# Optimization experiments

Hardware: AMD Instinct MI355X
Metric: run time of the kernel (lower is better)

Reference implementation:

```python
import jax, jax.numpy as jnp
import numpy as np

B, CIN, COUT, H, W = 8, 256, 256, 64, 64
WBIT = 4  # weight_bit


def _fake_quant_sym(w, bits):
    # Symmetric per-tensor fake quantization with straight-through rounding.
    n = 2.0 ** (bits - 1) - 1
    mag = jax.lax.stop_gradient(
        jnp.maximum(jnp.abs(jnp.min(w)), jnp.abs(jnp.max(w))))
    s = jnp.maximum(mag, 1e-8) / n
    q = w / s
    q = q + jax.lax.stop_gradient(jnp.round(q) - q)  # STE round
    return jnp.clip(q, -n - 1, n) * s


def _conv3x3(x, w, b):
    out = jax.lax.conv_general_dilated(
        x, w, window_strides=(1, 1), padding=((1, 1), (1, 1)),
        dimension_numbers=('NCHW', 'OIHW', 'NCHW'))
    return out + b[None, :, None, None]


def _bilinear_gather(x, py, px):
    # x: [B,C,H,W]; py, px: [B,K,Ho,Wo] float sample coords. Zero outside.
    b, c, h, w = x.shape
    y0 = jnp.floor(py)
    x0 = jnp.floor(px)
    wy = (py - y0)[:, None]  # [B,1,K,Ho,Wo]
    wx = (px - x0)[:, None]
    flat = x.reshape(b, c, h * w)

    def gather(yi, xi):
        valid = (yi >= 0) & (yi <= h - 1) & (xi >= 0) & (xi <= w - 1)
        yc = jnp.clip(yi, 0, h - 1).astype(jnp.int32)
        xc = jnp.clip(xi, 0, w - 1).astype(jnp.int32)
        idx = (yc * w + xc).reshape(b, -1)  # [B, K*Ho*Wo]
        g = jax.vmap(lambda f, i: f[:, i])(flat, idx)  # [B,C,K*Ho*Wo]
        g = g.reshape(b, c, *yi.shape[1:])  # [B,C,K,Ho,Wo]
        return g * valid[:, None].astype(x.dtype)

    v00 = gather(y0, x0)
    v01 = gather(y0, x0 + 1)
    v10 = gather(y0 + 1, x0)
    v11 = gather(y0 + 1, x0 + 1)
    return (v00 * (1 - wy) * (1 - wx) + v01 * (1 - wy) * wx
            + v10 * wy * (1 - wx) + v11 * wy * wx)


def setup_inputs() -> dict:
    key = jax.random.key(0)
    ks = jax.random.split(key, 4)
    return {
        'x': jax.random.normal(ks[0], (B, CIN, H, W), jnp.float32),
        'w_off': jax.random.normal(ks[1], (2, CIN, 3, 3), jnp.float32) * 0.01,
        'b_off': jnp.zeros((2,), jnp.float32),
        'w_scale': jax.random.normal(ks[2], (1, CIN, 3, 3), jnp.float32) * 0.01,
        'b_scale': jnp.ones((1,), jnp.float32),
        'w_dcn': jax.random.normal(ks[3], (COUT, CIN, 3, 3), jnp.float32)
                 / np.float32(np.sqrt(CIN * 9)),
        'b_dcn': jnp.zeros((COUT,), jnp.float32),
    }


def reference(x, w_off, b_off, w_scale, b_scale, w_dcn, b_dcn):
    # Fake-quantize all conv weights (per-tensor symmetric, STE).
    w_off_q = _fake_quant_sym(w_off, WBIT)
    w_scale_q = _fake_quant_sym(w_scale, WBIT)
    w_dcn_q = _fake_quant_sym(w_dcn, WBIT)

    # Per-location offset (dy,dx) and positive-bounded scale.
    off = _conv3x3(x, w_off_q, b_off)                 # [B,2,H,W]
    scale = jax.nn.relu(_conv3x3(x, w_scale_q, b_scale))  # [B,1,H,W]

    # Kernel anchor grid (row-major 3x3, (ry,rx) in {-1,0,1}).
    ry = jnp.array([-1, -1, -1, 0, 0, 0, 1, 1, 1], jnp.float32)
    rx = jnp.array([-1, 0, 1, -1, 0, 1, -1, 0, 1], jnp.float32)
    ii = jnp.arange(H, dtype=jnp.float32)[None, None, :, None]
    jj = jnp.arange(W, dtype=jnp.float32)[None, None, None, :]
    # sample pos = base + anchor + [offset + anchor*(scale-1)] = base + anchor*scale + offset
    py = ii + ry[None, :, None, None] * scale + off[:, 0:1]   # [B,9,H,W]
    px = jj + rx[None, :, None, None] * scale + off[:, 1:2]

    sampled = _bilinear_gather(x, py, px)             # [B,C,9,H,W]
    out = jnp.einsum('bckhw,ock->bohw', sampled, w_dcn_q.reshape(COUT, CIN, 9))
    return out + b_dcn[None, :, None, None]
```

## Files before the change

kernel.cpp:

```cpp
#include <hip/hip_runtime.h>

#define BB   8
#define CIN  256
#define COUT 256
#define HH   64
#define WW   64
#define HW   (HH*WW)
#define KT   9
#define KTOT (CIN*KT)
#define WR   12
#define RSTR 65
#define CSTR 786

typedef short short8 __attribute__((ext_vector_type(8)));
typedef float f32x4  __attribute__((ext_vector_type(4)));
typedef float f32x2  __attribute__((ext_vector_type(2)));
typedef float f32x16 __attribute__((ext_vector_type(16)));
union FragU { short8 s8; unsigned u[4]; uint4 u4; };

#define WS_OFF     0
#define WS_SCALE   65536
#define WS_PART    98304
#define WS_SDCN    98368
#define WS_WOFFQ   98372
#define WS_WSCALEQ 102980
#define WS_B       105284

#define USE_FP8_HW __has_builtin(__builtin_amdgcn_cvt_pk_f32_fp8)

__device__ __forceinline__ float fq(float w, float s) {
    float q = rintf(w / s);
    q = fminf(fmaxf(q, -8.f), 7.f);
    return q * s;
}

__device__ __forceinline__ unsigned short f2bf(float f) {
    unsigned u = __float_as_uint(f);
    return (unsigned short)((u + 0x7fffu + ((u >> 16) & 1u)) >> 16);
}

__global__ __launch_bounds__(256) void prep_kernel(const float* __restrict__ w_dcn,
                                                   const float* __restrict__ w_off,
                                                   const float* __restrict__ w_scale,
                                                   float* __restrict__ ws) {
    __shared__ float red[256];
    const int bx = blockIdx.x, tid = threadIdx.x;
    if (bx < 64) {
        float m = 0.f;
        const float* p = w_dcn + bx * 9216;
#pragma unroll
        for (int k = 0; k < 36; ++k) m = fmaxf(m, fabsf(p[tid + k * 256]));
        red[tid] = m;
        __syncthreads();
        for (int s = 128; s > 0; s >>= 1) {
            if (tid < s) red[tid] = fmaxf(red[tid], red[tid + s]);
            __syncthreads();
        }
        if (tid == 0) ws[WS_PART + bx] = red[0];
    } else {
        const float* src = (bx == 64) ? w_off : w_scale;
        const int n = (bx == 64) ? 2 * KTOT : KTOT;
        float* dst = ws + ((bx == 64) ? WS_WOFFQ : WS_WSCALEQ);
        float m = 0.f;
        for (int i = tid; i < n; i += 256) m = fmaxf(m, fabsf(src[i]));
        red[tid] = m;
        __syncthreads();
        for (int s = 128; s > 0; s >>= 1) {
            if (tid < s) red[tid] = fmaxf(red[tid], red[tid + s]);
            __syncthreads();
        }
        float sq = fmaxf(red[0], 1e-8f) / 7.f;
        for (int i = tid; i < n; i += 256) dst[i] = fq(src[i], sq);
    }
}

__global__ __launch_bounds__(256) void mid_kernel(const float* __restrict__ x,
                                                  const float* __restrict__ w_dcn,
                                                  float* __restrict__ ws) {
    __shared__ float R[4][3][64];
    const int bx = blockIdx.x, tid = threadIdx.x;
    if (bx < 512) {
        const int b = bx & 7, i = bx >> 3;
        const int j = tid & 63, cq = tid >> 6;
        const float* woq = ws + WS_WOFFQ;
        const float* wsq = ws + WS_WSCALEQ;
        float a0 = 0.f, a1 = 0.f, a2 = 0.f;
        for (int c = cq * 64; c < cq * 64 + 64; ++c) {
            const float* xb = x + (size_t)(b * CIN + c) * HW;
            const float* w0 = woq + c * 9;
            const float* w1 = woq + KTOT + c * 9;
            const float* w2 = wsq + c * 9;
#pragma unroll
            for (int di = -1; di <= 1; ++di) {
                int yy = i + di;
                bool rv = (yy >= 0) && (yy < HH);
#pragma unroll
                for (int dj = -1; dj <= 1; ++dj) {
                    int xx = j + dj;
                    float xv = (rv && xx >= 0 && xx < WW) ? xb[yy * WW + xx] : 0.f;
                    int t = (di + 1) * 3 + (dj + 1);
                    a0 += xv * w0[t];
                    a1 += xv * w1[t];
                    a2 += xv * w2[t];
                }
            }
        }
        R[cq][0][j] = a0; R[cq][1][j] = a1; R[cq][2][j] = a2;
        __syncthreads();
        if (tid < 192) {
            int comp = tid >> 6, j2 = tid & 63;
            float v = R[0][comp][j2] + R[1][comp][j2] +
                      R[2][comp][j2] + R[3][comp][j2];
            if (comp == 0)      ws[WS_OFF + (b * 2 + 0) * HW + i * WW + j2] = v;
            else if (comp == 1) ws[WS_OFF + (b * 2 + 1) * HW + i * WW + j2] = v;
            else                ws[WS_SCALE + b * HW + i * WW + j2] = v;
        }
    } else {
        const int qb = bx - 512;
        float m = 0.f;
#pragma unroll
        for (int k = 0; k < 64; ++k) m = fmaxf(m, ws[WS_PART + k]);
        float sd = fmaxf(m, 1e-8f) / 7.f;
        if (qb == 0 && tid == 0) ws[WS_SDCN] = sd;
        const int t4 = (qb * 256 + tid) * 4;
        float qv[4];
#pragma unroll
        for (int u = 0; u < 4; ++u) {
            int t = t4 + u;
            int j  = t & 7;
            int l  = (t >> 3) & 63;
            int nt = (t >> 9) & 7;
            int s  = t >> 12;
            int g = s / 10, r = s - g * 10;
            int p = r >> 1, o8 = r & 1;
            int ch = g * 16 + o8 * 8 + ((l >> 5) << 2) + (j >> 1);
            int tap = 2 * p + (j & 1);
            int o = nt * 32 + (l & 31);
            float w = (tap <= 8) ? w_dcn[(o * CIN + ch) * KT + tap] : 0.f;
            qv[u] = fminf(fmaxf(rintf(w / sd), -8.f), 7.f);
        }
        unsigned d;
#if USE_FP8_HW
        d = 0;
        d = __builtin_amdgcn_cvt_pk_fp8_f32(qv[0], qv[1], d, false);
        d = __builtin_amdgcn_cvt_pk_fp8_f32(qv[2], qv[3], d, true);
#else
        d = ((unsigned)(unsigned char)(signed char)(int)qv[0])
          | ((unsigned)(unsigned char)(signed char)(int)qv[1] << 8)
          | ((unsigned)(unsigned char)(signed char)(int)qv[2] << 16)
          | ((unsigned)(unsigned char)(signed char)(int)qv[3] << 24);
#endif
        ((unsigned*)(ws + WS_B))[qb * 256 + tid] = d;
    }
}

__device__ __forceinline__ void cvt4(unsigned d, unsigned& p0, unsigned& p1) {
#if USE_FP8_HW
    f32x2 lo = __builtin_amdgcn_cvt_pk_f32_fp8(d, false);
    f32x2 hi = __builtin_amdgcn_cvt_pk_f32_fp8(d, true);
    p0 = __builtin_amdgcn_perm(__float_as_uint(lo.y), __float_as_uint(lo.x),
                               0x07060302u);
    p1 = __builtin_amdgcn_perm(__float_as_uint(hi.y), __float_as_uint(hi.x),
                               0x07060302u);
#else
    float f0 = (float)(int)(signed char)(d & 0xff);
    float f1 = (float)(int)(signed char)((d >> 8) & 0xff);
    float f2 = (float)(int)(signed char)((d >> 16) & 0xff);
    float f3 = (float)(int)(signed char)(d >> 24);
    p0 = __builtin_amdgcn_perm(__float_as_uint(f1), __float_as_uint(f0),
                               0x07060302u);
    p1 = __builtin_amdgcn_perm(__float_as_uint(f3), __float_as_uint(f2),
                               0x07060302u);
#endif
}

__global__ __launch_bounds__(512, 4) void dcn_main_kernel(
    const float* __restrict__ x, const float* __restrict__ b_off,
    const float* __restrict__ b_scale, const float* __restrict__ b_dcn,
    const float* __restrict__ ws, float* __restrict__ out) {
    __shared__ unsigned sWin[16 * CSTR];
    __shared__ short8 sA[10][2][64];
    __shared__ int sRed[2];
    const int tid = threadIdx.x;
    const int bx = blockIdx.x;
    const int b = bx & 7;
    const int i = bx >> 3;
    const int w = tid >> 6, l = tid & 63;
    const int h = l >> 5;
    const int mtp = w & 1;
    const int colp = mtp * 32 + (l & 31);
    const int mtc = w & 1, ntp = w >> 1;
    const float* xb = x + (size_t)b * CIN * HW;
    const char* Bb = (const char*)(ws + WS_B);
    const float sdcn = ws[WS_SDCN];

    if (tid == 0) { sRed[0] = 64; sRed[1] = -1; }

    unsigned mRC[9], mW0[9], mW1[9];
    {
        float o0 = ws[WS_OFF + (b * 2 + 0) * HW + i * WW + colp] + b_off[0];
        float o1 = ws[WS_OFF + (b * 2 + 1) * HW + i * WW + colp] + b_off[1];
        float sc = fmaxf(ws[WS_SCALE + b * HW + i * WW + colp] + b_scale[0], 0.f);
        int rmn = 64, rmx = -1;
#pragma unroll
        for (int tap = 0; tap < 9; ++tap) {
            float ry = (float)(tap / 3 - 1), rx = (float)(tap % 3 - 1);
            float py = (float)i + ry * sc + o0;
            float px = (float)colp + rx * sc + o1;
            float y0f = floorf(py), x0f = floorf(px);
            float wy = py - y0f, wx = px - x0f;
            float w00 = (1.f - wy) * (1.f - wx), w01 = (1.f - wy) * wx;
            float w10 = wy * (1.f - wx),         w11 = wy * wx;
            bool vy0 = (y0f >= 0.f)  && (y0f <= 63.f);
            bool vy1 = (y0f >= -1.f) && (y0f <= 62.f);
            bool vx0 = (x0f >= 0.f)  && (x0f <= 63.f);
            bool vx1 = (x0f >= -1.f) && (x0f <= 62.f);
            bool d0hi = x0f > 62.f, d1lo = x0f < 0.f;
            float e0 = 0.f, e1 = 0.f, e2 = 0.f, e3 = 0.f;
            if (vy0 && vx0) { if (d0hi) e1 += w00; else e0 += w00; }
            if (vy0 && vx1) { if (d1lo) e0 += w01; else e1 += w01; }
            if (vy1 && vx0) { if (d0hi) e3 += w10; else e2 += w10; }
            if (vy1 && vx1) { if (d1lo) e2 += w11; else e3 += w11; }
            int r0 = (int)fminf(fmaxf(y0f, 0.f), 63.f);
            int r1 = (int)fminf(fmaxf(y0f + 1.f, 0.f), 63.f);
            int cb = (int)fminf(fmaxf(x0f, 0.f), 62.f);
            bool use0 = (e0 != 0.f) || (e1 != 0.f);
            bool use1 = (e2 != 0.f) || (e3 != 0.f);
            if (use0) { rmn = min(rmn, r0); rmx = max(rmx, r0); }
            if (use1) { rmn = min(rmn, r1); rmx = max(rmx, r1); }
            mRC[tap] = (unsigned)r0 | ((unsigned)r1 << 8) | ((unsigned)cb << 16) |
                       ((unsigned)use0 << 24) | ((unsigned)use1 << 25);
            mW0[tap] = (unsigned)f2bf(e0 * sdcn) | ((unsigned)f2bf(e1 * sdcn) << 16);
            mW1[tap] = (unsigned)f2bf(e2 * sdcn) | ((unsigned)f2bf(e3 * sdcn) << 16);
        }
        __syncthreads();
        atomicMin(&sRed[0], rmn);
        atomicMax(&sRed[1], rmx);
    }
    __syncthreads();
    const int rmin = sRed[0], rmax = sRed[1];
    const int rlo = min(max(rmin, 0), HH - WR);
    const bool fast = (rmax - rlo) <= (WR - 1);

    unsigned mOb[9];
#pragma unroll
    for (int tap = 0; tap < 9; ++tap) {
        unsigned rc = mRC[tap];
        int r0 = rc & 0xff, r1 = (rc >> 8) & 0xff, cb = (rc >> 16) & 0xff;
        int u0 = (rc >> 24) & 1, u1 = (rc >> 25) & 1;
        int a0, a1;
        if (fast) {
            a0 = ((u0 ? (r0 - rlo) : 0) * RSTR + cb) * 4;
            a1 = ((u1 ? (r1 - rlo) : 0) * RSTR + cb) * 4;
        } else {
            a0 = (r0 * WW + cb) * 4;
            a1 = (r1 * WW + cb) * 4;
        }
        mOb[tap] = (unsigned)a0 | ((unsigned)a1 << 16);
    }

    f32x16 acc0 = {0.f}, acc1 = {0.f};
#pragma unroll
    for (int r = 0; r < 16; ++r) { acc0[r] = 0.f; acc1[r] = 0.f; }

    auto produceUnit = [&](int g, int ksl, bool fastm) {
        const int p = ksl >> 1, o8 = ksl & 1;
        FragU af;
#pragma unroll
        for (int jc = 0; jc < 4; ++jc) {
            float vv0 = 0.f, vv1 = 0.f;
            const int chs = o8 * 8 + h * 4 + jc;
#pragma unroll
            for (int t = 0; t < 2; ++t) {
                int tap = 2 * p + t; if (tap > 8) tap = 8;
                unsigned ob = mOb[tap];
                float w00 = __uint_as_float(mW0[tap] << 16);
                float w01 = __uint_as_float(mW0[tap] & 0xffff0000u);
                float w10 = __uint_as_float(mW1[tap] << 16);
                float w11 = __uint_as_float(mW1[tap] & 0xffff0000u);
                float v;
                if (fastm) {
                    const char* base = (const char*)sWin + chs * (CSTR * 4);
                    unsigned dw0 = *(const unsigned*)(base + (ob & 0xffffu));
                    unsigned dw1 = *(const unsigned*)(base + (ob >> 16));
                    v = w00 * __uint_as_float(dw0 << 16) +
                        w01 * __uint_as_float(dw0 & 0xffff0000u) +
                        w10 * __uint_as_float(dw1 << 16) +
                        w11 * __uint_as_float(dw1 & 0xffff0000u);
                } else {
                    const char* pb = (const char*)(xb + (size_t)(g * 16 + chs) * HW);
                    float s0x = *(const float*)(pb + (ob & 0xffffu));
                    float s0y = *(const float*)(pb + (ob & 0xffffu) + 4);
                    float s1x = *(const float*)(pb + (ob >> 16));
                    float s1y = *(const float*)(pb + (ob >> 16) + 4);
                    v = w00 * s0x + w01 * s0y + w10 * s1x + w11 * s1y;
                }
                if (t == 0) vv0 = v; else vv1 = v;
            }
            af.u[jc] = (unsigned)f2bf(vv0) | ((unsigned)f2bf(vv1) << 16);
        }
        sA[ksl][mtp][l] = af.s8;
    };
    auto produceAll = [&](int g, bool fastm) {
        produceUnit(g, w >> 1, fastm);
        produceUnit(g, (w + 8) >> 1, fastm);
        if (w < 4) produceUnit(g, (w + 16) >> 1, fastm);
    };

    auto consumeStep = [&](int g, int ks) {
        const int s = g * 10 + ks;
        short8 af = sA[ks][mtc][l];
        const char* bp = Bb + ((size_t)(s * 8 + ntp * 2) * 64 + l) * 8;
        uint2 r0 = *(const uint2*)bp;
        uint2 r1 = *(const uint2*)(bp + 512);
        FragU b0, b1;
        cvt4(r0.x, b0.u[0], b0.u[1]); cvt4(r0.y, b0.u[2], b0.u[3]);
        cvt4(r1.x, b1.u[0], b1.u[1]); cvt4(r1.y, b1.u[2], b1.u[3]);
        acc0 = __builtin_amdgcn_mfma_f32_32x32x16_bf16(af, b0.s8, acc0, 0, 0, 0);
        acc1 = __builtin_amdgcn_mfma_f32_32x32x16_bf16(af, b1.s8, acc1, 0, 0, 0);
    };

    const int c4 = tid & 15;
    float4 sa[3]; float sb[3];
    auto stageLoad3 = [&](int g, int c0) {
#pragma unroll
        for (int c = 0; c < 3; ++c) {
            int id = tid + (c0 + c) * 512;
            int rowIdx = id >> 4;
            int ch = rowIdx / WR, rr = rowIdx - ch * WR;
            const float* src = xb + (size_t)(g * 16 + ch) * HW +
                               (rlo + rr) * WW + c4 * 4;
            sa[c] = *(const float4*)src;
            sb[c] = (c4 == 15) ? sa[c].w : src[4];
        }
    };
    auto stageWrite3 = [&](int c0) {
#pragma unroll
        for (int c = 0; c < 3; ++c) {
            int id = tid + (c0 + c) * 512;
            int rowIdx = id >> 4;
            int ch = rowIdx / WR, rr = rowIdx - ch * WR;
            unsigned* wp = &sWin[ch * CSTR + rr * RSTR + c4 * 4];
            float4 a = sa[c]; float b5 = sb[c];
            wp[0] = (unsigned)f2bf(a.x) | ((unsigned)f2bf(a.y) << 16);
            wp[1] = (unsigned)f2bf(a.y) | ((unsigned)f2bf(a.z) << 16);
            wp[2] = (unsigned)f2bf(a.z) | ((unsigned)f2bf(a.w) << 16);
            wp[3] = (unsigned)f2bf(a.w) | ((unsigned)f2bf(b5) << 16);
        }
    };

    if (fast) {
        stageLoad3(0, 0); stageWrite3(0);
        stageLoad3(0, 3); stageWrite3(3);
        __syncthreads();
        produceAll(0, true);
        __syncthreads();
        for (int g = 0; g < 16; ++g) {
            const bool hn = g < 15;
            if (hn) stageLoad3(g + 1, 0);
            consumeStep(g, 0); consumeStep(g, 1); consumeStep(g, 2);
            consumeStep(g, 3); consumeStep(g, 4);
            if (hn) { stageWrite3(0); stageLoad3(g + 1, 3); }
            consumeStep(g, 5); consumeStep(g, 6); consumeStep(g, 7);
            consumeStep(g, 8); consumeStep(g, 9);
            if (hn) stageWrite3(3);
            __syncthreads();
            if (hn) {
                produceAll(g + 1, true);
                __syncthreads();
            }
        }
    } else {
        for (int g = 0; g < 16; ++g) {
            produceAll(g, false);
            __syncthreads();
#pragma unroll
            for (int ks = 0; ks < 10; ++ks) consumeStep(g, ks);
            __syncthreads();
        }
    }

#pragma unroll
    for (int t = 0; t < 2; ++t) {
        f32x16 A = t ? acc1 : acc0;
        int o = (ntp * 2 + t) * 32 + (l & 31);
        float bb = b_dcn[o];
        float* ob = out + ((size_t)(b * COUT + o) * HH + i) * WW + mtc * 32 + 4 * h;
#pragma unroll
        for (int rq = 0; rq < 4; ++rq) {
            f32x4 v = {A[rq * 4 + 0] + bb, A[rq * 4 + 1] + bb,
                       A[rq * 4 + 2] + bb, A[rq * 4 + 3] + bb};
            *(f32x4*)(ob + rq * 8) = v;
        }
    }
}

extern "C" void kernel_launch(void* const* d_in, const int* in_sizes, int n_in,
                              void* d_out, int out_size, void* d_ws, size_t ws_size,
                              hipStream_t stream) {
    const float* x       = (const float*)d_in[0];
    const float* w_off   = (const float*)d_in[1];
    const float* b_off   = (const float*)d_in[2];
    const float* w_scale = (const float*)d_in[3];
    const float* b_scale = (const float*)d_in[4];
    const float* w_dcn   = (const float*)d_in[5];
    const float* b_dcn   = (const float*)d_in[6];
    float* out = (float*)d_out;
    float* ws  = (float*)d_ws;

    prep_kernel<<<dim3(66),   dim3(256), 0, stream>>>(w_dcn, w_off, w_scale, ws);
    mid_kernel <<<dim3(1152), dim3(256), 0, stream>>>(x, w_dcn, ws);
    dcn_main_kernel<<<dim3(512), dim3(512), 0, stream>>>(
        x, b_off, b_scale, b_dcn, ws, out);
}
```

Before: 285.7 us.

## Halve channel group size, stage weight quant through LDS, raise occupancy

The main DCN kernel now processes 8-channel groups (32 iterations) with a smaller LDS window and A-fragment buffer, and raises launch bounds from 4 to 6 waves per EU so more blocks fit per CU. The window gains zero-padded border rows so each tap needs only one row index, and bf16 packing uses a cheaper truncate-plus-round perm. Staging is simplified to load-then-write without register double-buffering across consume steps. The weight quantization part of mid_kernel stages contiguous w_dcn slices in shared memory to coalesce reads and cuts its grid from 1152 to 544 blocks. The trade-off is twice as many barriers and less overlap of global loads with MFMA work, plus a small rounding difference in the bf16 conversion.

```diff
diff --git a/kernel.cpp b/kernel.cpp
--- a/kernel.cpp
+++ b/kernel.cpp
@@ -10,7 +10,7 @@
 #define KTOT (CIN*KT)
 #define WR   12
 #define RSTR 65
-#define CSTR 786
+#define CSTR 911
 
 typedef short short8 __attribute__((ext_vector_type(8)));
 typedef float f32x4  __attribute__((ext_vector_type(4)));
@@ -37,6 +37,12 @@
 __device__ __forceinline__ unsigned short f2bf(float f) {
     unsigned u = __float_as_uint(f);
     return (unsigned short)((u + 0x7fffu + ((u >> 16) & 1u)) >> 16);
+}
+
+__device__ __forceinline__ unsigned pkbf(float a, float b) {
+    unsigned ua = __float_as_uint(a) + 0x8000u;
+    unsigned ub = __float_as_uint(b) + 0x8000u;
+    return __builtin_amdgcn_perm(ub, ua, 0x07060302u);
 }
 
 __global__ __launch_bounds__(256) void prep_kernel(const float* __restrict__ w_dcn,
@@ -78,6 +84,7 @@
                                                   const float* __restrict__ w_dcn,
                                                   float* __restrict__ ws) {
     __shared__ float R[4][3][64];
+    __shared__ float Wt[256 * 73];
     const int bx = blockIdx.x, tid = threadIdx.x;
     if (bx < 512) {
         const int b = bx & 7, i = bx >> 3;
@@ -116,41 +123,48 @@
             else                ws[WS_SCALE + b * HW + i * WW + j2] = v;
         }
     } else {
-        const int qb = bx - 512;
+        const int g = bx - 512;
         float m = 0.f;
 #pragma unroll
         for (int k = 0; k < 64; ++k) m = fmaxf(m, ws[WS_PART + k]);
         float sd = fmaxf(m, 1e-8f) / 7.f;
-        if (qb == 0 && tid == 0) ws[WS_SDCN] = sd;
-        const int t4 = (qb * 256 + tid) * 4;
-        float qv[4];
-#pragma unroll
-        for (int u = 0; u < 4; ++u) {
-            int t = t4 + u;
-            int j  = t & 7;
-            int l  = (t >> 3) & 63;
-            int nt = (t >> 9) & 7;
-            int s  = t >> 12;
-            int g = s / 10, r = s - g * 10;
-            int p = r >> 1, o8 = r & 1;
-            int ch = g * 16 + o8 * 8 + ((l >> 5) << 2) + (j >> 1);
-            int tap = 2 * p + (j & 1);
+        if (g == 0 && tid == 0) ws[WS_SDCN] = sd;
+        for (int f = tid; f < 256 * 72; f += 256) {
+            int o = f / 72, u = f - o * 72;
+            Wt[o * 73 + u] = w_dcn[o * KTOT + g * 72 + u];
+        }
+        __syncthreads();
+#pragma unroll 4
+        for (int rep = 0; rep < 20; ++rep) {
+            int fd = rep * 256 + tid;
+            int j4 = fd & 1;
+            int l  = (fd >> 1) & 63;
+            int nt = (fd >> 7) & 7;
+            int ks = fd >> 10;
+            int s = g * 5 + ks;
             int o = nt * 32 + (l & 31);
-            float w = (tap <= 8) ? w_dcn[(o * CIN + ch) * KT + tap] : 0.f;
-            qv[u] = fminf(fmaxf(rintf(w / sd), -8.f), 7.f);
-        }
-        unsigned d;
+            float qv[4];
+#pragma unroll
+            for (int jj = 0; jj < 4; ++jj) {
+                int j = j4 * 4 + jj;
+                int k16 = ((l >> 5) << 3) + j;
+                int tap = ks * 2 + (k16 & 1);
+                float wv = (tap <= 8) ? Wt[o * 73 + (k16 >> 1) * 9 + tap] : 0.f;
+                qv[jj] = fminf(fmaxf(rintf(wv / sd), -8.f), 7.f);
+            }
+            unsigned d;
 #if USE_FP8_HW
-        d = 0;
-        d = __builtin_amdgcn_cvt_pk_fp8_f32(qv[0], qv[1], d, false);
-        d = __builtin_amdgcn_cvt_pk_fp8_f32(qv[2], qv[3], d, true);
+            d = 0;
+            d = __builtin_amdgcn_cvt_pk_fp8_f32(qv[0], qv[1], d, false);
+            d = __builtin_amdgcn_cvt_pk_fp8_f32(qv[2], qv[3], d, true);
 #else
-        d = ((unsigned)(unsigned char)(signed char)(int)qv[0])
-          | ((unsigned)(unsigned char)(signed char)(int)qv[1] << 8)
-          | ((unsigned)(unsigned char)(signed char)(int)qv[2] << 16)
-          | ((unsigned)(unsigned char)(signed char)(int)qv[3] << 24);
+            d = ((unsigned)(unsigned char)(signed char)(int)qv[0])
+              | ((unsigned)(unsigned char)(signed char)(int)qv[1] << 8)
+              | ((unsigned)(unsigned char)(signed char)(int)qv[2] << 16)
+              | ((unsigned)(unsigned char)(signed char)(int)qv[3] << 24);
 #endif
-        ((unsigned*)(ws + WS_B))[qb * 256 + tid] = d;
+            ((unsigned*)(ws + WS_B))[((s * 8 + nt) * 64 + l) * 2 + j4] = d;
+        }
     }
 }
 
@@ -174,22 +188,21 @@
 #endif
 }
 
-__global__ __launch_bounds__(512, 4) void dcn_main_kernel(
+__global__ __launch_bounds__(512, 6) void dcn_main_kernel(
     const float* __restrict__ x, const float* __restrict__ b_off,
     const float* __restrict__ b_scale, const float* __restrict__ b_dcn,
     const float* __restrict__ ws, float* __restrict__ out) {
-    __shared__ unsigned sWin[16 * CSTR];
-    __shared__ short8 sA[10][2][64];
+    __shared__ unsigned sWin[8 * CSTR];
+    __shared__ short8 sA[5][2][64];
     __shared__ int sRed[2];
     const int tid = threadIdx.x;
     const int bx = blockIdx.x;
     const int b = bx & 7;
     const int i = bx >> 3;
     const int w = tid >> 6, l = tid & 63;
-    const int h = l >> 5;
-    const int mtp = w & 1;
-    const int colp = mtp * 32 + (l & 31);
+    const int h = l >> 5, ln31 = l & 31;
     const int mtc = w & 1, ntp = w >> 1;
+    const int colp = mtc * 32 + ln31;
     const float* xb = x + (size_t)b * CIN * HW;
     const char* Bb = (const char*)(ws + WS_B);
     const float sdcn = ws[WS_SDCN];
@@ -242,140 +255,133 @@
     const int rlo = min(max(rmin, 0), HH - WR);
     const bool fast = (rmax - rlo) <= (WR - 1);
 
-    unsigned mOb[9];
+    int aoff[9];
 #pragma unroll
     for (int tap = 0; tap < 9; ++tap) {
         unsigned rc = mRC[tap];
         int r0 = rc & 0xff, r1 = (rc >> 8) & 0xff, cb = (rc >> 16) & 0xff;
         int u0 = (rc >> 24) & 1, u1 = (rc >> 25) & 1;
-        int a0, a1;
-        if (fast) {
-            a0 = ((u0 ? (r0 - rlo) : 0) * RSTR + cb) * 4;
-            a1 = ((u1 ? (r1 - rlo) : 0) * RSTR + cb) * 4;
-        } else {
-            a0 = (r0 * WW + cb) * 4;
-            a1 = (r1 * WW + cb) * 4;
-        }
-        mOb[tap] = (unsigned)a0 | ((unsigned)a1 << 16);
-    }
-
-    f32x16 acc0 = {0.f}, acc1 = {0.f};
+        int ridx = u0 ? (r0 - rlo + 1) : (u1 ? (r1 - rlo) : 0);
+        aoff[tap] = ridx * RSTR + cb;
+    }
+
+    f32x16 acc0, acc1;
 #pragma unroll
     for (int r = 0; r < 16; ++r) { acc0[r] = 0.f; acc1[r] = 0.f; }
 
-    auto produceUnit = [&](int g, int ksl, bool fastm) {
-        const int p = ksl >> 1, o8 = ksl & 1;
-        FragU af;
-#pragma unroll
-        for (int jc = 0; jc < 4; ++jc) {
-            float vv0 = 0.f, vv1 = 0.f;
-            const int chs = o8 * 8 + h * 4 + jc;
+    auto produceFast = [&](int g) {
+        (void)g;
+#pragma unroll
+        for (int u = 0; u < 5; ++u) {
+            int qf = ntp * 5 + u;
+            int ksl = qf >> 2, jc = qf & 3;
+            int chl = h * 4 + jc;
+            const unsigned* slot = sWin + chl * CSTR;
+            const unsigned* p = slot + aoff[2 * ksl];
+            unsigned dw0 = p[0], dw1 = p[RSTR];
+            float w00 = __uint_as_float(mW0[2 * ksl] << 16);
+            float w01 = __uint_as_float(mW0[2 * ksl] & 0xffff0000u);
+            float w10 = __uint_as_float(mW1[2 * ksl] << 16);
+            float w11 = __uint_as_float(mW1[2 * ksl] & 0xffff0000u);
+            float v0 = w00 * __uint_as_float(dw0 << 16) +
+                       w01 * __uint_as_float(dw0 & 0xffff0000u) +
+                       w10 * __uint_as_float(dw1 << 16) +
+                       w11 * __uint_as_float(dw1 & 0xffff0000u);
+            float v1 = 0.f;
+            if (ksl < 4) {
+                const unsigned* q = slot + aoff[2 * ksl + 1];
+                unsigned dq0 = q[0], dq1 = q[RSTR];
+                float z00 = __uint_as_float(mW0[2 * ksl + 1] << 16);
+                float z01 = __uint_as_float(mW0[2 * ksl + 1] & 0xffff0000u);
+                float z10 = __uint_as_float(mW1[2 * ksl + 1] << 16);
+                float z11 = __uint_as_float(mW1[2 * ksl + 1] & 0xffff0000u);
+                v1 = z00 * __uint_as_float(dq0 << 16) +
+                     z01 * __uint_as_float(dq0 & 0xffff0000u) +
+                     z10 * __uint_as_float(dq1 << 16) +
+                     z11 * __uint_as_float(dq1 & 0xffff0000u);
+            }
+            ((unsigned*)&sA[ksl][mtc][l])[jc] = pkbf(v0, v1);
+        }
+    };
+    auto produceSlow = [&](int g) {
+#pragma unroll
+        for (int u = 0; u < 5; ++u) {
+            int qf = ntp * 5 + u;
+            int ksl = qf >> 2, jc = qf & 3;
+            int chl = h * 4 + jc;
+            const float* pl = xb + (size_t)(g * 8 + chl) * HW;
+            float vv[2];
 #pragma unroll
             for (int t = 0; t < 2; ++t) {
-                int tap = 2 * p + t; if (tap > 8) tap = 8;
-                unsigned ob = mOb[tap];
+                int tap = 2 * ksl + t;
+                if (tap > 8) { vv[t] = 0.f; continue; }
+                unsigned rc = mRC[tap];
+                int r0 = rc & 0xff, r1 = (rc >> 8) & 0xff, cb = (rc >> 16) & 0xff;
                 float w00 = __uint_as_float(mW0[tap] << 16);
                 float w01 = __uint_as_float(mW0[tap] & 0xffff0000u);
                 float w10 = __uint_as_float(mW1[tap] << 16);
                 float w11 = __uint_as_float(mW1[tap] & 0xffff0000u);
-                float v;
-                if (fastm) {
-                    const char* base = (const char*)sWin + chs * (CSTR * 4);
-                    unsigned dw0 = *(const unsigned*)(base + (ob & 0xffffu));
-                    unsigned dw1 = *(const unsigned*)(base + (ob >> 16));
-                    v = w00 * __uint_as_float(dw0 << 16) +
-                        w01 * __uint_as_float(dw0 & 0xffff0000u) +
-                        w10 * __uint_as_float(dw1 << 16) +
-                        w11 * __uint_as_float(dw1 & 0xffff0000u);
-                } else {
-                    const char* pb = (const char*)(xb + (size_t)(g * 16 + chs) * HW);
-                    float s0x = *(const float*)(pb + (ob & 0xffffu));
-                    float s0y = *(const float*)(pb + (ob & 0xffffu) + 4);
-                    float s1x = *(const float*)(pb + (ob >> 16));
-                    float s1y = *(const float*)(pb + (ob >> 16) + 4);
-                    v = w00 * s0x + w01 * s0y + w10 * s1x + w11 * s1y;
-                }
-                if (t == 0) vv0 = v; else vv1 = v;
+                const float* p0 = pl + r0 * WW + cb;
+                const float* p1 = pl + r1 * WW + cb;
+                vv[t] = w00 * p0[0] + w01 * p0[1] + w10 * p1[0] + w11 * p1[1];
             }
-            af.u[jc] = (unsigned)f2bf(vv0) | ((unsigned)f2bf(vv1) << 16);
-        }
-        sA[ksl][mtp][l] = af.s8;
+            ((unsigned*)&sA[ksl][mtc][l])[jc] = pkbf(vv[0], vv[1]);
+        }
     };
-    auto produceAll = [&](int g, bool fastm) {
-        produceUnit(g, w >> 1, fastm);
-        produceUnit(g, (w + 8) >> 1, fastm);
-        if (w < 4) produceUnit(g, (w + 16) >> 1, fastm);
+
+    auto consume = [&](int g) {
+        const char* bp = Bb + ((size_t)(g * 5 * 8 + ntp * 2) * 64 + l) * 8;
+#pragma unroll
+        for (int ks = 0; ks < 5; ++ks) {
+            uint2 ra = *(const uint2*)(bp + ks * 4096);
+            uint2 rb = *(const uint2*)(bp + ks * 4096 + 512);
+            FragU b0, b1;
+            cvt4(ra.x, b0.u[0], b0.u[1]); cvt4(ra.y, b0.u[2], b0.u[3]);
+            cvt4(rb.x, b1.u[0], b1.u[1]); cvt4(rb.y, b1.u[2], b1.u[3]);
+            short8 af = sA[ks][mtc][l];
+            acc0 = __builtin_amdgcn_mfma_f32_32x32x16_bf16(af, b0.s8, acc0, 0, 0, 0);
+            acc1 = __builtin_amdgcn_mfma_f32_32x32x16_bf16(af, b1.s8, acc1, 0, 0, 0);
+        }
     };
 
-    auto consumeStep = [&](int g, int ks) {
-        const int s = g * 10 + ks;
-        short8 af = sA[ks][mtc][l];
-        const char* bp = Bb + ((size_t)(s * 8 + ntp * 2) * 64 + l) * 8;
-        uint2 r0 = *(const uint2*)bp;
-        uint2 r1 = *(const uint2*)(bp + 512);
-        FragU b0, b1;
-        cvt4(r0.x, b0.u[0], b0.u[1]); cvt4(r0.y, b0.u[2], b0.u[3]);
-        cvt4(r1.x, b1.u[0], b1.u[1]); cvt4(r1.y, b1.u[2], b1.u[3]);
-        acc0 = __builtin_amdgcn_mfma_f32_32x32x16_bf16(af, b0.s8, acc0, 0, 0, 0);
-        acc1 = __builtin_amdgcn_mfma_f32_32x32x16_bf16(af, b1.s8, acc1, 0, 0, 0);
+    auto stage = [&](int g) {
+        const int seg = l & 15;
+#pragma unroll
+        for (int c = 0; c < 3; ++c) {
+            int row = (l >> 4) + c * 4;
+            const float* src = xb + (size_t)(g * 8 + w) * HW +
+                               (rlo + row) * WW + seg * 4;
+            float4 a = *(const float4*)src;
+            float b5 = (seg == 15) ? a.w : src[4];
+            unsigned* wp = &sWin[w * CSTR + (row + 1) * RSTR + seg * 4];
+            wp[0] = pkbf(a.x, a.y);
+            wp[1] = pkbf(a.y, a.z);
+            wp[2] = pkbf(a.z, a.w);
+            wp[3] = pkbf(a.w, b5);
+        }
     };
 
-    const int c4 = tid & 15;
-    float4 sa[3]; float sb[3];
-    auto stageLoad3 = [&](int g, int c0) {
-#pragma unroll
-        for (int c = 0; c < 3; ++c) {
-            int id = tid + (c0 + c) * 512;
-            int rowIdx = id >> 4;
-            int ch = rowIdx / WR, rr = rowIdx - ch * WR;
-            const float* src = xb + (size_t)(g * 16 + ch) * HW +
-                               (rlo + rr) * WW + c4 * 4;
-            sa[c] = *(const float4*)src;
-            sb[c] = (c4 == 15) ? sa[c].w : src[4];
-        }
-    };
-    auto stageWrite3 = [&](int c0) {
-#pragma unroll
-        for (int c = 0; c < 3; ++c) {
-            int id = tid + (c0 + c) * 512;
-            int rowIdx = id >> 4;
-            int ch = rowIdx / WR, rr = rowIdx - ch * WR;
-            unsigned* wp = &sWin[ch * CSTR + rr * RSTR + c4 * 4];
-            float4 a = sa[c]; float b5 = sb[c];
-            wp[0] = (unsigned)f2bf(a.x) | ((unsigned)f2bf(a.y) << 16);
-            wp[1] = (unsigned)f2bf(a.y) | ((unsigned)f2bf(a.z) << 16);
-            wp[2] = (unsigned)f2bf(a.z) | ((unsigned)f2bf(a.w) << 16);
-            wp[3] = (unsigned)f2bf(a.w) | ((unsigned)f2bf(b5) << 16);
-        }
-    };
-
     if (fast) {
-        stageLoad3(0, 0); stageWrite3(0);
-        stageLoad3(0, 3); stageWrite3(3);
-        __syncthreads();
-        produceAll(0, true);
-        __syncthreads();
-        for (int g = 0; g < 16; ++g) {
-            const bool hn = g < 15;
-            if (hn) stageLoad3(g + 1, 0);
-            consumeStep(g, 0); consumeStep(g, 1); consumeStep(g, 2);
-            consumeStep(g, 3); consumeStep(g, 4);
-            if (hn) { stageWrite3(0); stageLoad3(g + 1, 3); }
-            consumeStep(g, 5); consumeStep(g, 6); consumeStep(g, 7);
-            consumeStep(g, 8); consumeStep(g, 9);
-            if (hn) stageWrite3(3);
-            __syncthreads();
-            if (hn) {
-                produceAll(g + 1, true);
-                __syncthreads();
-            }
+        for (int e = tid; e < 8 * 130; e += 512) {
+            int c = e / 130, r = e - c * 130;
+            sWin[c * CSTR + (r < 65 ? r : 13 * RSTR + (r - 65))] = 0u;
+        }
+        stage(0);
+        __syncthreads();
+        produceFast(0);
+        __syncthreads();
+        for (int g = 0; g < 32; ++g) {
+            consume(g);
+            if (g < 31) stage(g + 1);
+            __syncthreads();
+            if (g < 31) produceFast(g + 1);
+            __syncthreads();
         }
     } else {
-        for (int g = 0; g < 16; ++g) {
-            produceAll(g, false);
-            __syncthreads();
-#pragma unroll
-            for (int ks = 0; ks < 10; ++ks) consumeStep(g, ks);
+        for (int g = 0; g < 32; ++g) {
+            produceSlow(g);
+            __syncthreads();
+            consume(g);
             __syncthreads();
         }
     }
@@ -383,7 +389,7 @@
 #pragma unroll
     for (int t = 0; t < 2; ++t) {
         f32x16 A = t ? acc1 : acc0;
-        int o = (ntp * 2 + t) * 32 + (l & 31);
+        int o = (ntp * 2 + t) * 32 + ln31;
         float bb = b_dcn[o];
         float* ob = out + ((size_t)(b * COUT + o) * HH + i) * WW + mtc * 32 + 4 * h;
 #pragma unroll
@@ -408,8 +414,8 @@
     float* out = (float*)d_out;
     float* ws  = (float*)d_ws;
 
-    prep_kernel<<<dim3(66),   dim3(256), 0, stream>>>(w_dcn, w_off, w_scale, ws);
-    mid_kernel <<<dim3(1152), dim3(256), 0, stream>>>(x, w_dcn, ws);
+    prep_kernel<<<dim3(66),  dim3(256), 0, stream>>>(w_dcn, w_off, w_scale, ws);
+    mid_kernel <<<dim3(544), dim3(256), 0, stream>>>(x, w_dcn, ws);
     dcn_main_kernel<<<dim3(512), dim3(512), 0, stream>>>(
         x, b_off, b_scale, b_dcn, ws, out);
 }
```

Measured after the change: 647.7 us. +126.7%, slower.
